# Optimization experiments

Measured on AMD Instinct MI355X. Metric: run time of the kernel, lower is better.

Reference implementation:

```python
import jax, jax.numpy as jnp
import numpy as np

N_POINTS = 100000
N_PAIRS = 50000   # pairs per kernel offset
K_OFFSETS = 27    # 3^3 kernel offsets for 3D kernel_size=3
C = 128


def setup_inputs() -> dict:
    key = jax.random.key(0)
    ks = jax.random.split(key, 7)
    features = jax.random.normal(ks[0], (N_POINTS, C), dtype=jnp.float32)
    in_map = jax.random.randint(ks[1], (K_OFFSETS, N_PAIRS), 0, N_POINTS)
    out_map = jax.random.randint(ks[2], (K_OFFSETS, N_PAIRS), 0, N_POINTS)
    # scale weights so two stacked convs stay numerically tame in fp32
    W0 = jax.random.normal(ks[3], (K_OFFSETS, C, C), dtype=jnp.float32) * 0.05
    b0 = jax.random.normal(ks[4], (C,), dtype=jnp.float32)
    W1 = jax.random.normal(ks[5], (K_OFFSETS, C, C), dtype=jnp.float32) * 0.05
    b1 = jax.random.normal(ks[6], (C,), dtype=jnp.float32)
    return {"features": features, "in_map": in_map, "out_map": out_map,
            "W0": W0, "b0": b0, "W1": W1, "b1": b1}


def _sparse_conv(x, W, b, in_map, out_map, n_out):
    """Minkowski-style sparse conv: gather -> per-offset matmul -> scatter-add.
    x: [N, C], W: [K, C, C], in_map/out_map: [K, P]."""
    gathered = x[in_map]                                  # [K, P, C]
    msg = jnp.einsum('kpc,kcd->kpd', gathered, W)         # [K, P, C]
    y = jax.ops.segment_sum(msg.reshape(-1, msg.shape[-1]),
                            out_map.reshape(-1),
                            num_segments=n_out)           # [N, C]
    return y + b


def reference(features, in_map, out_map, W0, b0, W1, b1):
    n = features.shape[0]
    out = jax.nn.relu(_sparse_conv(features, W0, b0, in_map, out_map, n))
    out = _sparse_conv(out, W1, b1, in_map, out_map, n)
    return out + features
```

## Files before the change

kernel.cpp:

```cpp
#include <hip/hip_runtime.h>

#define N_POINTS 100000
#define N_PAIRS  50000
#define K_OFFSETS 27
#define C 128
#define WPAD 136
#define CAP 48

typedef __attribute__((ext_vector_type(8))) short short8;
typedef __attribute__((ext_vector_type(4))) float floatx4;

__device__ inline unsigned short f2bf(float f) {
  unsigned int u = __float_as_uint(f);
  return (unsigned short)((u + 0x7FFFu + ((u >> 16) & 1u)) >> 16);
}
__device__ inline float bf2f(unsigned int lo16) {
  return __uint_as_float(lo16 << 16);
}

__global__ __launch_bounds__(256) void prep_w_kernel(
    const float* __restrict__ W0, const float* __restrict__ W1,
    unsigned short* __restrict__ WT0, unsigned short* __restrict__ WT1) {
  int i = blockIdx.x * 256 + threadIdx.x;
  const int per = K_OFFSETS * C * C;
  if (i >= 2 * per) return;
  const float* W = (i < per) ? W0 : W1;
  unsigned short* WT = (i < per) ? WT0 : WT1;
  int r = (i < per) ? i : i - per;
  int k = r / (C * C);
  int q = r % (C * C);
  int d = q / C;
  int c = q % C;
  WT[k * C * C + d * C + c] = f2bf(W[k * C * C + c * C + d]);
}

__global__ __launch_bounds__(256) void prep_x_kernel(
    const float* __restrict__ features, const float* __restrict__ b0,
    unsigned short* __restrict__ xb, float* __restrict__ out, int write_out) {
  int i = (blockIdx.x * 256 + threadIdx.x) * 4;
  if (i >= N_POINTS * C) return;
  float4 f = *(const float4*)&features[i];
  ushort4 u;
  u.x = f2bf(f.x); u.y = f2bf(f.y); u.z = f2bf(f.z); u.w = f2bf(f.w);
  *(ushort4*)&xb[i] = u;
  if (write_out) {
    float4 b = *(const float4*)&b0[i & 127];
    *(float4*)&out[i] = b;
  }
}

__global__ __launch_bounds__(256) void zero_counts_kernel(int* __restrict__ counts) {
  int i = blockIdx.x * 256 + threadIdx.x;
  if (i < N_POINTS) counts[i] = 0;
}

__global__ __launch_bounds__(256) void build_csr_kernel(
    const int* __restrict__ out_map, int* __restrict__ counts, int* __restrict__ idxbuf) {
  int base = (blockIdx.x * 256 + threadIdx.x) * 4;
  if (base >= K_OFFSETS * N_PAIRS) return;
  int4 o4 = *(const int4*)&out_map[base];
  int o[4] = {o4.x, o4.y, o4.z, o4.w};
  int pos[4];
#pragma unroll
  for (int j = 0; j < 4; ++j) pos[j] = atomicAdd(&counts[o[j]], 1);
#pragma unroll
  for (int j = 0; j < 4; ++j) {
    int flat = base + j;
    int k = flat / N_PAIRS;
    int p = flat - k * N_PAIRS;
    if (pos[j] < CAP) idxbuf[o[j] * CAP + pos[j]] = (k << 16) | p;
  }
}

__global__ __launch_bounds__(256, 4) void conv_msg_kernel(
    const unsigned short* __restrict__ xb, const unsigned short* __restrict__ wbt,
    const int* __restrict__ in_map, unsigned short* __restrict__ msg, int k0) {
  __shared__ unsigned short Wlds[C * WPAD];

  const int k = k0 + blockIdx.y;
  const int pairBase = blockIdx.x * 128;
  const int tid = threadIdx.x;

  const unsigned short* wk = wbt + k * C * C;
#pragma unroll
  for (int it = 0; it < 8; ++it) {
    int t = tid + it * 256;
    int row = t >> 4;
    int col = (t & 15) << 3;
    *(uint4*)&Wlds[row * WPAD + col] = *(const uint4*)&wk[row * C + col];
  }
  __syncthreads();

  const int wave = tid >> 6;
  const int lane = tid & 63;
  const int l15 = lane & 15;
  const int kg = lane >> 4;
  const int pair0 = pairBase + wave * 32;

  const int prA0 = pair0 + l15;
  const int prA1 = pair0 + 16 + l15;
  const int inIdx0 = (prA0 < N_PAIRS) ? in_map[k * N_PAIRS + prA0] : 0;
  const int inIdx1 = (prA1 < N_PAIRS) ? in_map[k * N_PAIRS + prA1] : 0;
  const unsigned short* arow0 = xb + (size_t)inIdx0 * C + kg * 8;
  const unsigned short* arow1 = xb + (size_t)inIdx1 * C + kg * 8;

  floatx4 acc0[8], acc1[8];
#pragma unroll
  for (int nt = 0; nt < 8; ++nt) {
    acc0[nt] = (floatx4){0.f, 0.f, 0.f, 0.f};
    acc1[nt] = (floatx4){0.f, 0.f, 0.f, 0.f};
  }

#pragma unroll
  for (int kk = 0; kk < 4; ++kk) {
    short8 a0 = *(const short8*)(arow0 + kk * 32);
    short8 a1 = *(const short8*)(arow1 + kk * 32);
    const unsigned short* bbase = &Wlds[l15 * WPAD + kk * 32 + kg * 8];
#pragma unroll
    for (int nt = 0; nt < 8; ++nt) {
      short8 b = *(const short8*)(bbase + nt * 16 * WPAD);
      acc0[nt] = __builtin_amdgcn_mfma_f32_16x16x32_bf16(a0, b, acc0[nt], 0, 0, 0);
      acc1[nt] = __builtin_amdgcn_mfma_f32_16x16x32_bf16(a1, b, acc1[nt], 0, 0, 0);
    }
  }

#pragma unroll
  for (int i = 0; i < 4; ++i) {
    int pr0 = pair0 + kg * 4 + i;
    if (pr0 < N_PAIRS) {
      unsigned short* row = msg + (size_t)(blockIdx.y * N_PAIRS + pr0) * C;
      uint4 v;
      v.x = (unsigned int)f2bf(acc0[0][i]) | ((unsigned int)f2bf(acc0[1][i]) << 16);
      v.y = (unsigned int)f2bf(acc0[2][i]) | ((unsigned int)f2bf(acc0[3][i]) << 16);
      v.z = (unsigned int)f2bf(acc0[4][i]) | ((unsigned int)f2bf(acc0[5][i]) << 16);
      v.w = (unsigned int)f2bf(acc0[6][i]) | ((unsigned int)f2bf(acc0[7][i]) << 16);
      *(uint4*)(row + l15 * 8) = v;
    }
    int pr1 = pair0 + 16 + kg * 4 + i;
    if (pr1 < N_PAIRS) {
      unsigned short* row = msg + (size_t)(blockIdx.y * N_PAIRS + pr1) * C;
      uint4 v;
      v.x = (unsigned int)f2bf(acc1[0][i]) | ((unsigned int)f2bf(acc1[1][i]) << 16);
      v.y = (unsigned int)f2bf(acc1[2][i]) | ((unsigned int)f2bf(acc1[3][i]) << 16);
      v.z = (unsigned int)f2bf(acc1[4][i]) | ((unsigned int)f2bf(acc1[5][i]) << 16);
      v.w = (unsigned int)f2bf(acc1[6][i]) | ((unsigned int)f2bf(acc1[7][i]) << 16);
      *(uint4*)(row + l15 * 8) = v;
    }
  }
}

__global__ __launch_bounds__(256) void gather_kernel(
    const unsigned short* __restrict__ msg, const int* __restrict__ counts,
    const int* __restrict__ idxbuf, const float* __restrict__ bias,
    const float* __restrict__ features, float* __restrict__ out,
    unsigned short* __restrict__ x1b,
    int k0, int G, int init_mode, int fin_mode) {
  __shared__ int elds[4][64];
  const int wave = threadIdx.x >> 6;
  const int lane = threadIdx.x & 63;
  const int oi = blockIdx.x * 4 + wave;

  const int c0 = ((2 * lane) & 7) * 16 + (lane >> 2);
  const int c1 = c0 + 16;
  const size_t base = (size_t)oi * C;

  float a0, a1;
  if (init_mode == 1)      { a0 = bias[c0]; a1 = bias[c1]; }
  else if (init_mode == 2) { a0 = bias[c0] + features[base + c0];
                             a1 = bias[c1] + features[base + c1]; }
  else                     { a0 = out[base + c0]; a1 = out[base + c1]; }

  int cnt = counts[oi]; if (cnt > CAP) cnt = CAP;

  int e_mine = (lane < cnt) ? idxbuf[oi * CAP + lane] : 0;
  bool ok = false;
  if (lane < cnt) {
    unsigned int rel = ((unsigned int)e_mine >> 16) - (unsigned int)k0;
    ok = rel < (unsigned int)G;
  }
  unsigned long long mask = __ballot(ok);
  int cnt2 = __popcll(mask);
  if (ok) {
    int pos = __popcll(mask & ((1ull << lane) - 1ull));
    unsigned int rel = ((unsigned int)e_mine >> 16) - (unsigned int)k0;
    elds[wave][pos] = (int)(rel * N_PAIRS + ((unsigned int)e_mine & 0xffffu));
  }
  __syncthreads();

  const unsigned short* mbase = msg + 2 * lane;
  int t = 0;
  for (; t + 4 <= cnt2; t += 4) {
    int f0 = elds[wave][t];
    int f1 = elds[wave][t + 1];
    int f2 = elds[wave][t + 2];
    int f3 = elds[wave][t + 3];
    unsigned int v0 = *(const unsigned int*)(mbase + (size_t)f0 * C);
    unsigned int v1 = *(const unsigned int*)(mbase + (size_t)f1 * C);
    unsigned int v2 = *(const unsigned int*)(mbase + (size_t)f2 * C);
    unsigned int v3 = *(const unsigned int*)(mbase + (size_t)f3 * C);
    a0 += bf2f(v0 & 0xffffu) + bf2f(v1 & 0xffffu) + bf2f(v2 & 0xffffu) + bf2f(v3 & 0xffffu);
    a1 += bf2f(v0 >> 16) + bf2f(v1 >> 16) + bf2f(v2 >> 16) + bf2f(v3 >> 16);
  }
  for (; t < cnt2; ++t) {
    int f0 = elds[wave][t];
    unsigned int v = *(const unsigned int*)(mbase + (size_t)f0 * C);
    a0 += bf2f(v & 0xffffu);
    a1 += bf2f(v >> 16);
  }

  if (fin_mode == 1) {
    x1b[base + c0] = f2bf(fmaxf(a0, 0.f));
    x1b[base + c1] = f2bf(fmaxf(a1, 0.f));
  } else {
    out[base + c0] = a0;
    out[base + c1] = a1;
  }
}

__global__ __launch_bounds__(256) void mid_kernel(
    const float* __restrict__ features, const float* __restrict__ b1,
    float* __restrict__ out, unsigned short* __restrict__ x1b) {
  int i = (blockIdx.x * 256 + threadIdx.x) * 4;
  if (i >= N_POINTS * C) return;
  float4 y = *(const float4*)&out[i];
  ushort4 u;
  u.x = f2bf(fmaxf(y.x, 0.f));
  u.y = f2bf(fmaxf(y.y, 0.f));
  u.z = f2bf(fmaxf(y.z, 0.f));
  u.w = f2bf(fmaxf(y.w, 0.f));
  *(ushort4*)&x1b[i] = u;
  float4 f = *(const float4*)&features[i];
  float4 b = *(const float4*)&b1[i & 127];
  float4 o;
  o.x = f.x + b.x; o.y = f.y + b.y; o.z = f.z + b.z; o.w = f.w + b.w;
  *(float4*)&out[i] = o;
}

__global__ __launch_bounds__(256, 4) void conv_atomic_kernel(
    const unsigned short* __restrict__ xb, const unsigned short* __restrict__ wbt,
    const int* __restrict__ in_map, const int* __restrict__ out_map,
    float* __restrict__ out) {
  __shared__ unsigned short Wlds[C * WPAD];
  const int k = blockIdx.y;
  const int pairBase = blockIdx.x * 64;
  const int tid = threadIdx.x;
  const unsigned short* wk = wbt + k * C * C;
#pragma unroll
  for (int it = 0; it < 8; ++it) {
    int t = tid + it * 256;
    int row = t >> 4;
    int col = (t & 15) << 3;
    *(uint4*)&Wlds[row * WPAD + col] = *(const uint4*)&wk[row * C + col];
  }
  __syncthreads();
  const int wave = tid >> 6;
  const int lane = tid & 63;
  const int l15 = lane & 15;
  const int kg = lane >> 4;
  const int pair0 = pairBase + wave * 16;
  const int prA = pair0 + l15;
  const int inIdx = (prA < N_PAIRS) ? in_map[k * N_PAIRS + prA] : 0;
  const unsigned short* arow = xb + (size_t)inIdx * C + kg * 8;
  floatx4 acc[8];
#pragma unroll
  for (int nt = 0; nt < 8; ++nt) acc[nt] = (floatx4){0.f, 0.f, 0.f, 0.f};
#pragma unroll
  for (int kk = 0; kk < 4; ++kk) {
    short8 a = *(const short8*)(arow + kk * 32);
    const unsigned short* bbase = &Wlds[l15 * WPAD + kk * 32 + kg * 8];
#pragma unroll
    for (int nt = 0; nt < 8; ++nt) {
      short8 b = *(const short8*)(bbase + nt * 16 * WPAD);
      acc[nt] = __builtin_amdgcn_mfma_f32_16x16x32_bf16(a, b, acc[nt], 0, 0, 0);
    }
  }
#pragma unroll
  for (int i = 0; i < 4; ++i) {
    int pr = pair0 + kg * 4 + i;
    if (pr < N_PAIRS) {
      int oi = out_map[k * N_PAIRS + pr];
      float* orow = out + (size_t)oi * C + l15;
#pragma unroll
      for (int nt = 0; nt < 8; ++nt) atomicAdd(orow + nt * 16, acc[nt][i]);
    }
  }
}

extern "C" void kernel_launch(void* const* d_in, const int* in_sizes, int n_in,
                              void* d_out, int out_size, void* d_ws, size_t ws_size,
                              hipStream_t stream) {
  const float* features = (const float*)d_in[0];
  const int* in_map     = (const int*)d_in[1];
  const int* out_map    = (const int*)d_in[2];
  const float* W0       = (const float*)d_in[3];
  const float* b0       = (const float*)d_in[4];
  const float* W1       = (const float*)d_in[5];
  const float* b1       = (const float*)d_in[6];
  float* out = (float*)d_out;

  char* ws = (char*)d_ws;
  unsigned short* xb  = (unsigned short*)(ws);
  unsigned short* x1b = (unsigned short*)(ws + 25600000);
  unsigned short* WT0 = (unsigned short*)(ws + 51200000);
  unsigned short* WT1 = (unsigned short*)(ws + 52084736);
  int* counts         = (int*)(ws + 52969472);
  int* idxbuf         = (int*)(ws + 53369856);
  unsigned short* msg = (unsigned short*)(ws + 72569856);

  const long long MSG_K_BYTES = (long long)N_PAIRS * C * 2;
  long long avail = (long long)ws_size - 72569856LL;
  int G = 0;
  if (avail >= MSG_K_BYTES) {
    long long g = avail / MSG_K_BYTES;
    G = (int)(g > K_OFFSETS ? K_OFFSETS : g);
  }

  prep_w_kernel<<<(2 * K_OFFSETS * C * C + 255) / 256, 256, 0, stream>>>(W0, W1, WT0, WT1);
  prep_x_kernel<<<(N_POINTS * C / 4 + 255) / 256, 256, 0, stream>>>(
      features, b0, xb, out, (G > 0) ? 0 : 1);

  if (G > 0) {
    zero_counts_kernel<<<(N_POINTS + 255) / 256, 256, 0, stream>>>(counts);
    build_csr_kernel<<<(K_OFFSETS * N_PAIRS / 4 + 255) / 256, 256, 0, stream>>>(out_map, counts, idxbuf);

    const int nchunks = (K_OFFSETS + G - 1) / G;
    for (int layer = 0; layer < 2; ++layer) {
      const unsigned short* xin = layer ? x1b : xb;
      const unsigned short* wt  = layer ? WT1 : WT0;
      const float* bias         = layer ? b1  : b0;
      for (int c = 0; c < nchunks; ++c) {
        int k0 = c * G;
        int Gc = K_OFFSETS - k0 < G ? K_OFFSETS - k0 : G;
        dim3 cgrid((N_PAIRS + 127) / 128, Gc);
        conv_msg_kernel<<<cgrid, 256, 0, stream>>>(xin, wt, in_map, msg, k0);
        int init_mode = (c == 0) ? (layer ? 2 : 1) : 0;
        int fin_mode  = (layer == 0 && c == nchunks - 1) ? 1 : 0;
        gather_kernel<<<N_POINTS / 4, 256, 0, stream>>>(
            msg, counts, idxbuf, bias, features, out, x1b, k0, Gc, init_mode, fin_mode);
      }
    }
  } else {
    dim3 cgrid((N_PAIRS + 63) / 64, K_OFFSETS);
    conv_atomic_kernel<<<cgrid, 256, 0, stream>>>(xb, WT0, in_map, out_map, out);
    mid_kernel<<<(N_POINTS * C / 4 + 255) / 256, 256, 0, stream>>>(features, b1, out, x1b);
    conv_atomic_kernel<<<cgrid, 256, 0, stream>>>(x1b, WT1, in_map, out_map, out);
  }
}
```

Before: 719.5 us.

## Build per-output CSR via two-pass binning with LDS-local lists

Replaces the per-point global atomic CSR build with a two-pass scheme. The first pass bins pairs into 128-point buckets, split across two sub-buffers to reduce atomic contention. The second pass builds each bucket's per-point lists with shared-memory atomics and writes them to idxbuf with coalesced int4 stores. This targets scattered global atomics and uncoalesced idxbuf writes, at the cost of an extra kernel and a staging buffer that reuses the msg workspace. Buckets overflowing BCAP would silently drop pairs.

```diff
diff --git a/kernel.cpp b/kernel.cpp
--- a/kernel.cpp
+++ b/kernel.cpp
@@ -6,6 +6,10 @@
 #define C 128
 #define WPAD 136
 #define CAP 48
+
+#define PPB 128
+#define NB  782
+#define BCAP 1152
 
 typedef __attribute__((ext_vector_type(8))) short short8;
 typedef __attribute__((ext_vector_type(4))) float floatx4;
@@ -49,26 +53,68 @@
   }
 }
 
-__global__ __launch_bounds__(256) void zero_counts_kernel(int* __restrict__ counts) {
+__global__ __launch_bounds__(256) void zero_bcnt_kernel(int* __restrict__ bcnt) {
   int i = blockIdx.x * 256 + threadIdx.x;
-  if (i < N_POINTS) counts[i] = 0;
-}
-
-__global__ __launch_bounds__(256) void build_csr_kernel(
-    const int* __restrict__ out_map, int* __restrict__ counts, int* __restrict__ idxbuf) {
-  int base = (blockIdx.x * 256 + threadIdx.x) * 4;
+  if (i < 2 * NB) bcnt[i] = 0;
+}
+
+__global__ __launch_bounds__(256) void bin_pass1_kernel(
+    const int* __restrict__ out_map, int* __restrict__ bcnt, int* __restrict__ binbuf) {
+  int t = blockIdx.x * 256 + threadIdx.x;
+  int base = t * 4;
   if (base >= K_OFFSETS * N_PAIRS) return;
   int4 o4 = *(const int4*)&out_map[base];
   int o[4] = {o4.x, o4.y, o4.z, o4.w};
-  int pos[4];
-#pragma unroll
-  for (int j = 0; j < 4; ++j) pos[j] = atomicAdd(&counts[o[j]], 1);
+  const int s = t & 1;
+  int* cnt = bcnt + s * NB;
+  int* buf = binbuf + s * (NB * BCAP);
+  int b[4], pos[4];
+#pragma unroll
+  for (int j = 0; j < 4; ++j) b[j] = o[j] >> 7;
+#pragma unroll
+  for (int j = 0; j < 4; ++j) pos[j] = atomicAdd(&cnt[b[j]], 1);
 #pragma unroll
   for (int j = 0; j < 4; ++j) {
     int flat = base + j;
     int k = flat / N_PAIRS;
     int p = flat - k * N_PAIRS;
-    if (pos[j] < CAP) idxbuf[o[j] * CAP + pos[j]] = (k << 16) | p;
+    if (pos[j] < BCAP)
+      buf[b[j] * BCAP + pos[j]] = ((o[j] & (PPB - 1)) << 21) | (k << 16) | p;
+  }
+}
+
+__global__ __launch_bounds__(256) void bin_pass2_kernel(
+    const int* __restrict__ bcnt, const int* __restrict__ binbuf,
+    int* __restrict__ counts, int* __restrict__ idxbuf) {
+  __shared__ int lists[PPB][CAP];
+  __shared__ int lcnt[PPB];
+  const int b = blockIdx.x;
+  const int tid = threadIdx.x;
+  if (tid < PPB) lcnt[tid] = 0;
+  __syncthreads();
+#pragma unroll
+  for (int s = 0; s < 2; ++s) {
+    int bc = bcnt[s * NB + b]; if (bc > BCAP) bc = BCAP;
+    const int* seg = binbuf + s * (NB * BCAP) + b * BCAP;
+    for (int t = tid; t < bc; t += 256) {
+      int e = seg[t];
+      int lo = ((unsigned int)e) >> 21;
+      int pos = atomicAdd(&lcnt[lo], 1);
+      if (pos < CAP) lists[lo][pos] = e & 0x1FFFFF;
+    }
+  }
+  __syncthreads();
+  const int o0 = b * PPB;
+  if (tid < PPB) {
+    int o = o0 + tid;
+    if (o < N_POINTS) counts[o] = lcnt[tid];
+  }
+  for (int c = tid; c < PPB * CAP / 4; c += 256) {
+    int lo = c / (CAP / 4);
+    int slot = (c - lo * (CAP / 4)) * 4;
+    int o = o0 + lo;
+    if (o < N_POINTS)
+      *(int4*)&idxbuf[(size_t)o * CAP + slot] = *(const int4*)&lists[lo][slot];
   }
 }
 
@@ -306,6 +352,8 @@
   int* counts         = (int*)(ws + 52969472);
   int* idxbuf         = (int*)(ws + 53369856);
   unsigned short* msg = (unsigned short*)(ws + 72569856);
+  int* binbuf = (int*)(ws + 72569856);
+  int* bcnt   = (int*)(ws + 72569856 + 2 * NB * BCAP * 4);
 
   const long long MSG_K_BYTES = (long long)N_PAIRS * C * 2;
   long long avail = (long long)ws_size - 72569856LL;
@@ -320,8 +368,10 @@
       features, b0, xb, out, (G > 0) ? 0 : 1);
 
   if (G > 0) {
-    zero_counts_kernel<<<(N_POINTS + 255) / 256, 256, 0, stream>>>(counts);
-    build_csr_kernel<<<(K_OFFSETS * N_PAIRS / 4 + 255) / 256, 256, 0, stream>>>(out_map, counts, idxbuf);
+    zero_bcnt_kernel<<<(2 * NB + 255) / 256, 256, 0, stream>>>(bcnt);
+    bin_pass1_kernel<<<(K_OFFSETS * N_PAIRS / 4 + 255) / 256, 256, 0, stream>>>(
+        out_map, bcnt, binbuf);
+    bin_pass2_kernel<<<NB, 256, 0, stream>>>(bcnt, binbuf, counts, idxbuf);
 
     const int nchunks = (K_OFFSETS + G - 1) / G;
     for (int layer = 0; layer < 2; ++layer) {
```

After: 804.8 us. 1.12x slower.
